# Optimization experiments

Hardware: AMD Instinct MI355X
Metric: run time of the kernel (lower is better)

Reference implementation:

```python
import jax, jax.numpy as jnp
import numpy as np

D_MODEL = 1024
NUM_HEADS = 16
NUM_KV_HEADS = 4
HEAD_DIM = D_MODEL // NUM_HEADS  # 64
THETA = 10000.0
MAX_SEQ_LEN = 4096


def _rope_tables(max_seq_len, d_k, theta):
    k_vec = jnp.arange(0, d_k, 2, dtype=jnp.float32) / d_k
    freq = 1.0 / (theta ** k_vec)                       # (d_k/2,)
    ang = jnp.arange(max_seq_len, dtype=jnp.float32)[:, None] * freq[None, :]
    return jnp.cos(ang), jnp.sin(ang)                   # each (max_seq_len, d_k/2)


def _apply_rope(x, pos, cos_table, sin_table):
    # x: (b, h, l, d), pos: (b, l)
    cos = cos_table[pos][:, None, :, :]                 # (b, 1, l, d/2)
    sin = sin_table[pos][:, None, :, :]
    even, odd = x[..., 0::2], x[..., 1::2]
    r1 = even * cos - odd * sin
    r2 = even * sin + odd * cos
    return jnp.stack([r1, r2], axis=-1).reshape(x.shape)  # interleave back


def setup_inputs() -> dict:
    key = jax.random.key(0)
    ks = jax.random.split(key, 6)
    B, L, D = 1, 4096, D_MODEL
    std = (2.0 / (D + D)) ** 0.5
    std_kv = (2.0 / (D + HEAD_DIM * NUM_KV_HEADS)) ** 0.5
    x = jax.random.normal(ks[0], (B, L, D), dtype=jnp.float32)
    Wq = jax.random.normal(ks[1], (D, D), dtype=jnp.float32) * std
    Wk = jax.random.normal(ks[2], (HEAD_DIM * NUM_KV_HEADS, D), dtype=jnp.float32) * std_kv
    Wv = jax.random.normal(ks[3], (HEAD_DIM * NUM_KV_HEADS, D), dtype=jnp.float32) * std_kv
    Wo = jax.random.normal(ks[4], (D, D), dtype=jnp.float32) * std
    token_positions = jnp.broadcast_to(jnp.arange(L, dtype=jnp.int32), (B, L))
    return {"x": x, "Wq": Wq, "Wk": Wk, "Wv": Wv, "Wo": Wo,
            "token_positions": token_positions}


def reference(x, Wq, Wk, Wv, Wo, token_positions):
    B, L, D = x.shape
    H, Hkv, Dh = NUM_HEADS, NUM_KV_HEADS, HEAD_DIM
    n_rep = H // Hkv
    cos_t, sin_t = _rope_tables(MAX_SEQ_LEN, Dh, THETA)

    q = (x @ Wq.T).reshape(B, L, H, Dh).transpose(0, 2, 1, 3)      # b h l d
    k = (x @ Wk.T).reshape(B, L, Hkv, Dh).transpose(0, 2, 1, 3)    # b g l d
    v = (x @ Wv.T).reshape(B, L, Hkv, Dh).transpose(0, 2, 1, 3)

    q = _apply_rope(q, token_positions, cos_t, sin_t)
    k = _apply_rope(k, token_positions, cos_t, sin_t)

    # GQA: group query heads by kv head
    qg = q.reshape(B, Hkv, n_rep, L, Dh)
    scores = jnp.einsum('bgrqd,bgkd->bgrqk', qg, k) / jnp.sqrt(jnp.float32(Dh))
    causal = jnp.tril(jnp.ones((L, L), dtype=bool))
    scores = jnp.where(causal, scores, -jnp.inf)
    weights = jax.nn.softmax(scores, axis=-1)
    out = jnp.einsum('bgrqk,bgkd->bgrqd', weights, v)              # b g r q d
    out = out.reshape(B, H, L, Dh).transpose(0, 2, 1, 3).reshape(B, L, D)
    return out @ Wo.T
```

## Files before the change

### kernel.cpp

```cpp
#include <hip/hip_runtime.h>
#include <hip/hip_bf16.h>
#include <math.h>

typedef __bf16 bf16;
typedef __bf16 v8bf __attribute__((ext_vector_type(8)));
typedef __bf16 v4bf __attribute__((ext_vector_type(4)));
typedef __bf16 v2bf __attribute__((ext_vector_type(2)));
typedef float f32x4 __attribute__((ext_vector_type(4)));
typedef float f32x16 __attribute__((ext_vector_type(16)));

#define L_SEQ 4096
#define DMODEL 1024
#define NHEADS 16
#define DH 64
#define NEG_BIG (-1e30f)
#define LN1E4_64 0.14391156f
#define SCL2 0.18033688f
#define DEFER_THR 8.0f

static __device__ __forceinline__ unsigned pkbf(float x, float y) {
    v2bf t; t[0] = (bf16)x; t[1] = (bf16)y;
    return __builtin_bit_cast(unsigned, t);
}

static __device__ __forceinline__ void gld16(const bf16* g, const bf16* l) {
    __builtin_amdgcn_global_load_lds((const __attribute__((address_space(1))) void*)g,
                                     (__attribute__((address_space(3))) void*)l, 16, 0, 0);
}

__global__ void convert_all(const float* __restrict__ x, const float* __restrict__ wq,
                            const float* __restrict__ wk, const float* __restrict__ wv,
                            const float* __restrict__ wo,
                            bf16* __restrict__ xb, bf16* __restrict__ wqkvb,
                            bf16* __restrict__ wob) {
    int i = (blockIdx.x * 256 + threadIdx.x) * 4;
    const float* src;
    bf16* dst;
    if (i < 4194304)      { src = x  + i;             dst = xb    + i; }
    else if (i < 5242880) { src = wq + (i - 4194304); dst = wqkvb + (i - 4194304); }
    else if (i < 5505024) { src = wk + (i - 5242880); dst = wqkvb + 1048576 + (i - 5242880); }
    else if (i < 5767168) { src = wv + (i - 5505024); dst = wqkvb + 1310720 + (i - 5505024); }
    else                  { src = wo + (i - 5767168); dst = wob   + (i - 5767168); }
    f32x4 v = *(const f32x4*)src;
    v4bf r;
#pragma unroll
    for (int j = 0; j < 4; j++) r[j] = (bf16)v[j];
    *(v4bf*)dst = r;
}

__global__ __launch_bounds__(512) void gemm_qkv(const bf16* __restrict__ A,
                                                const bf16* __restrict__ W,
                                                bf16* __restrict__ Qb,
                                                bf16* __restrict__ Kb,
                                                bf16* __restrict__ Vtg,
                                                const int* __restrict__ tp) {
    __shared__ bf16 As[2][128][64];
    __shared__ bf16 Bs[2][128][64];
    const int K = 1024;
    const int tid = threadIdx.x;
    const int w = tid >> 6, lane = tid & 63;
    const int quad = lane >> 4, l16 = lane & 15;
    const int wm = (w & 1) * 64, wn = (w >> 1) * 32;
    const int bm = blockIdx.x * 128, bn = blockIdx.y * 128;

    const int srow = lane >> 3;
    const int scol = ((lane & 7) ^ srow) << 3;

    f32x4 acc[4][2];
#pragma unroll
    for (int mf = 0; mf < 4; mf++)
#pragma unroll
        for (int nf = 0; nf < 2; nf++) acc[mf][nf] = (f32x4){0.f, 0.f, 0.f, 0.f};

#define QKV_STAGE(buf, ktt)                                                        \
    do {                                                                           \
        const bf16* ga = &A[(size_t)(bm + (w << 3) + srow) * 1024 + (ktt) + scol]; \
        const bf16* gb = &W[(size_t)(bn + (w << 3) + srow) * 1024 + (ktt) + scol]; \
        gld16(ga,             &As[buf][(w << 3)][0]);                              \
        gld16(ga + 64 * 1024, &As[buf][64 + (w << 3)][0]);                         \
        gld16(gb,             &Bs[buf][(w << 3)][0]);                              \
        gld16(gb + 64 * 1024, &Bs[buf][64 + (w << 3)][0]);                         \
    } while (0)

    QKV_STAGE(0, 0);
    __syncthreads();

    int cur = 0;
    for (int kt = 0; kt < K; kt += 64) {
        const bool more = (kt + 64) < K;
        if (more) QKV_STAGE(cur ^ 1, kt + 64);
#pragma unroll
        for (int kf = 0; kf < 2; kf++) {
            v8bf a[4], b[2];
#pragma unroll
            for (int mf = 0; mf < 4; mf++)
                a[mf] = *(v8bf*)&As[cur][wm + mf * 16 + l16][(((kf << 2) + quad) ^ (l16 & 7)) << 3];
#pragma unroll
            for (int nf = 0; nf < 2; nf++)
                b[nf] = *(v8bf*)&Bs[cur][wn + nf * 16 + l16][(((kf << 2) + quad) ^ (l16 & 7)) << 3];
#pragma unroll
            for (int mf = 0; mf < 4; mf++)
#pragma unroll
                for (int nf = 0; nf < 2; nf++)
                    acc[mf][nf] = __builtin_amdgcn_mfma_f32_16x16x32_bf16(a[mf], b[nf], acc[mf][nf], 0, 0, 0);
        }
        __syncthreads();
        cur ^= 1;
    }
#undef QKV_STAGE

    if (bn < 1024) {
#pragma unroll
        for (int mf = 0; mf < 4; mf++) {
            int pos_[4];
#pragma unroll
            for (int r = 0; r < 4; r++) pos_[r] = tp[bm + wm + mf * 16 + quad * 4 + r];
#pragma unroll
            for (int nf = 0; nf < 2; nf++) {
                const int col = bn + wn + nf * 16 + l16;
                float fr = __expf(-(float)((col & 63) & ~1) * LN1E4_64);
#pragma unroll
                for (int r = 0; r < 4; r++) {
                    float v = acc[mf][nf][r];
                    float sn, cs;
                    __sincosf((float)pos_[r] * fr, &sn, &cs);
                    float p = __shfl_xor(v, 1);
                    float res = (l16 & 1) ? (p * sn + v * cs) : (v * cs - p * sn);
                    int row = bm + wm + mf * 16 + quad * 4 + r;
                    Qb[(size_t)row * DMODEL + col] = (bf16)(res * SCL2);
                }
            }
        }
    } else if (bn < 1280) {
#pragma unroll
        for (int mf = 0; mf < 4; mf++) {
            int pos_[4];
#pragma unroll
            for (int r = 0; r < 4; r++) pos_[r] = tp[bm + wm + mf * 16 + quad * 4 + r];
#pragma unroll
            for (int nf = 0; nf < 2; nf++) {
                const int kcol = bn - 1024 + wn + nf * 16 + l16;
                float fr = __expf(-(float)((kcol & 63) & ~1) * LN1E4_64);
#pragma unroll
                for (int r = 0; r < 4; r++) {
                    float v = acc[mf][nf][r];
                    float sn, cs;
                    __sincosf((float)pos_[r] * fr, &sn, &cs);
                    float p = __shfl_xor(v, 1);
                    float res = (l16 & 1) ? (p * sn + v * cs) : (v * cs - p * sn);
                    int row = bm + wm + mf * 16 + quad * 4 + r;
                    Kb[(size_t)row * 256 + kcol] = (bf16)res;
                }
            }
        }
    } else {
#pragma unroll
        for (int mf = 0; mf < 4; mf++)
#pragma unroll
            for (int nf = 0; nf < 2; nf++) {
                v4bf pk;
#pragma unroll
                for (int r = 0; r < 4; r++) pk[r] = (bf16)acc[mf][nf][r];
                int vcol = bn - 1280 + wn + nf * 16 + l16;
                int row = bm + wm + mf * 16 + quad * 4;
                *(v4bf*)&Vtg[(size_t)vcol * L_SEQ + row] = pk;
            }
    }
}

__global__ __launch_bounds__(512) void gemm_out(const bf16* __restrict__ A,
                                                const bf16* __restrict__ W,
                                                float* __restrict__ C) {
    __shared__ bf16 As[2][128][64];
    __shared__ bf16 Bs[2][128][64];
    const int K = 1024, N = 1024;
    const int tid = threadIdx.x;
    const int w = tid >> 6, lane = tid & 63;
    const int quad = lane >> 4, l16 = lane & 15;
    const int wm = (w & 1) * 64, wn = (w >> 1) * 32;
    const int bm = blockIdx.x * 128, bn = blockIdx.y * 128;

    const int srow = lane >> 3;
    const int scol = ((lane & 7) ^ srow) << 3;

    f32x4 acc[4][2];
#pragma unroll
    for (int mf = 0; mf < 4; mf++)
#pragma unroll
        for (int nf = 0; nf < 2; nf++) acc[mf][nf] = (f32x4){0.f, 0.f, 0.f, 0.f};

#define OUT_STAGE(buf, ktt)                                                        \
    do {                                                                           \
        const bf16* ga = &A[(size_t)(bm + (w << 3) + srow) * 1024 + (ktt) + scol]; \
        const bf16* gb = &W[(size_t)(bn + (w << 3) + srow) * 1024 + (ktt) + scol]; \
        gld16(ga,             &As[buf][(w << 3)][0]);                              \
        gld16(ga + 64 * 1024, &As[buf][64 + (w << 3)][0]);                         \
        gld16(gb,             &Bs[buf][(w << 3)][0]);                              \
        gld16(gb + 64 * 1024, &Bs[buf][64 + (w << 3)][0]);                         \
    } while (0)

    OUT_STAGE(0, 0);
    __syncthreads();

    int cur = 0;
    for (int kt = 0; kt < K; kt += 64) {
        const bool more = (kt + 64) < K;
        if (more) OUT_STAGE(cur ^ 1, kt + 64);
#pragma unroll
        for (int kf = 0; kf < 2; kf++) {
            v8bf a[4], b[2];
#pragma unroll
            for (int mf = 0; mf < 4; mf++)
                a[mf] = *(v8bf*)&As[cur][wm + mf * 16 + l16][(((kf << 2) + quad) ^ (l16 & 7)) << 3];
#pragma unroll
            for (int nf = 0; nf < 2; nf++)
                b[nf] = *(v8bf*)&Bs[cur][wn + nf * 16 + l16][(((kf << 2) + quad) ^ (l16 & 7)) << 3];
#pragma unroll
            for (int mf = 0; mf < 4; mf++)
#pragma unroll
                for (int nf = 0; nf < 2; nf++)
                    acc[mf][nf] = __builtin_amdgcn_mfma_f32_16x16x32_bf16(a[mf], b[nf], acc[mf][nf], 0, 0, 0);
        }
        __syncthreads();
        cur ^= 1;
    }
#undef OUT_STAGE

#pragma unroll
    for (int mf = 0; mf < 4; mf++)
#pragma unroll
        for (int nf = 0; nf < 2; nf++)
#pragma unroll
            for (int r = 0; r < 4; r++) {
                int row = bm + wm + mf * 16 + quad * 4 + r;
                int col = bn + wn + nf * 16 + l16;
                C[(size_t)row * N + col] = acc[mf][nf][r];
            }
}

__global__ __launch_bounds__(256, 2) void flash11(const bf16* __restrict__ Q,
                                                  const bf16* __restrict__ Kb,
                                                  const bf16* __restrict__ Vtg,
                                                  bf16* __restrict__ O0,
                                                  bf16* __restrict__ O1,
                                                  float* __restrict__ ML) {
    __shared__ bf16 Ks[128][68];
    __shared__ bf16 Vt[64][132];
    const int h = blockIdx.x, kvh = h >> 2;
    const int bx = blockIdx.y;
    const int tid = threadIdx.x;
    const int w = tid >> 6, lane = tid & 63;
    const int l32 = lane & 31, hi = lane >> 5;
    const int krow = tid >> 1, kcb = (tid & 1) * 32;
    const int vr = tid >> 2, vcb = (tid & 3) * 32;

    v8bf ones;
#pragma unroll
    for (int j = 0; j < 8; j++) ones[j] = (bf16)1.0f;

    for (int p = 0; p < 2; p++) {
        const int qb = p ? (31 - bx) : bx;
        const int T = qb + 1;
        const int k0 = p ? ((T + 1) >> 1) : 0;
        const int k1 = p ? T : ((T + 1) >> 1);
        bf16* Op = p ? O1 : O0;
        float* mlp = ML + (size_t)(p * NHEADS + h) * L_SEQ * 2;

        if (k0 >= k1) {
            for (int i = tid; i < 128 * 64; i += 256) {
                int rr = i >> 6, cc = i & 63;
                Op[(size_t)(qb * 128 + rr) * DMODEL + h * DH + cc] = (bf16)0.f;
            }
            if (tid < 128) {
                mlp[(qb * 128 + tid) * 2 + 0] = NEG_BIG;
                mlp[(qb * 128 + tid) * 2 + 1] = 0.f;
            }
            continue;
        }

        const int qrow = qb * 128 + w * 32 + l32;
        v8bf qf[4];
#pragma unroll
        for (int d16 = 0; d16 < 4; d16++)
            qf[d16] = *(const v8bf*)&Q[(size_t)qrow * DMODEL + h * DH + d16 * 16 + hi * 8];

        f32x16 oaccT[2], lacc;
#pragma unroll
        for (int d = 0; d < 2; d++)
#pragma unroll
            for (int r = 0; r < 16; r++) oaccT[d][r] = 0.f;
#pragma unroll
        for (int r = 0; r < 16; r++) lacc[r] = 0.f;
        float m_i = NEG_BIG;

        v8bf kreg[4], vreg[4];
        {
            const bf16* ks = &Kb[(size_t)(k0 * 128 + krow) * 256 + kvh * DH + kcb];
            const bf16* vs = &Vtg[(size_t)(kvh * DH + vr) * L_SEQ + k0 * 128 + vcb];
#pragma unroll
            for (int u = 0; u < 4; u++) { kreg[u] = *(const v8bf*)&ks[8 * u]; vreg[u] = *(const v8bf*)&vs[8 * u]; }
            __syncthreads();
#pragma unroll
            for (int u = 0; u < 4; u++) { *(v8bf*)&Ks[krow][kcb + 8 * u] = kreg[u]; *(v8bf*)&Vt[vr][vcb + 8 * u] = vreg[u]; }
        }

        for (int kb = k0; kb < k1; kb++) {
            __syncthreads();
            if (kb + 1 < k1) {
                const bf16* ks = &Kb[(size_t)((kb + 1) * 128 + krow) * 256 + kvh * DH + kcb];
                const bf16* vs = &Vtg[(size_t)(kvh * DH + vr) * L_SEQ + (kb + 1) * 128 + vcb];
#pragma unroll
                for (int u = 0; u < 4; u++) { kreg[u] = *(const v8bf*)&ks[8 * u]; vreg[u] = *(const v8bf*)&vs[8 * u]; }
            }

            f32x16 s[4];
            __builtin_amdgcn_s_setprio(1);
#pragma unroll
            for (int n = 0; n < 4; n++) {
#pragma unroll
                for (int r = 0; r < 16; r++) s[n][r] = 0.f;
#pragma unroll
                for (int d16 = 0; d16 < 4; d16++) {
                    v8bf av = *(v8bf*)&Ks[n * 32 + l32][d16 * 16 + hi * 8];
                    s[n] = __builtin_amdgcn_mfma_f32_32x32x16_bf16(av, qf[d16], s[n], 0, 0, 0);
                }
            }
            __builtin_amdgcn_s_setprio(0);

            if (kb == qb) {
#pragma unroll
                for (int n = 0; n < 4; n++) {
                    int kbase = kb * 128 + n * 32 + 4 * hi;
#pragma unroll
                    for (int r = 0; r < 16; r++) {
                        int key = kbase + (r & 3) + 8 * (r >> 2);
                        if (key > qrow) s[n][r] = NEG_BIG;
                    }
                }
            }

            float mx = NEG_BIG;
#pragma unroll
            for (int n = 0; n < 4; n++)
#pragma unroll
                for (int r = 0; r < 16; r += 2)
                    mx = fmaxf(fmaxf(mx, s[n][r]), s[n][r + 1]);
            mx = fmaxf(mx, __shfl_xor(mx, 32));

            if (!__all(mx <= m_i + DEFER_THR)) {
                float mnew = fmaxf(m_i, mx);
                float alpha = exp2f(m_i - mnew);
#pragma unroll
                for (int r = 0; r < 16; r++) lacc[r] *= alpha;
#pragma unroll
                for (int d = 0; d < 2; d++)
#pragma unroll
                    for (int r = 0; r < 16; r++) oaccT[d][r] *= alpha;
                m_i = mnew;
            }

#pragma unroll
            for (int n = 0; n < 4; n++)
#pragma unroll
                for (int r = 0; r < 16; r++)
                    s[n][r] = exp2f(s[n][r] - m_i);

            __builtin_amdgcn_s_setprio(1);
#pragma unroll
            for (int n = 0; n < 4; n++) {
#pragma unroll
                for (int u = 0; u < 2; u++) {
                    const int ro = u * 8;
                    unsigned a0 = pkbf(s[n][ro + 0], s[n][ro + 1]);
                    unsigned a1 = pkbf(s[n][ro + 2], s[n][ro + 3]);
                    unsigned b0 = pkbf(s[n][ro + 4], s[n][ro + 5]);
                    unsigned b1 = pkbf(s[n][ro + 6], s[n][ro + 7]);
#if __has_builtin(__builtin_amdgcn_permlane32_swap)
                    auto s0 = __builtin_amdgcn_permlane32_swap(a0, b0, false, false);
                    auto s1 = __builtin_amdgcn_permlane32_swap(a1, b1, false, false);
                    unsigned w0 = s0[0], w2 = s0[1], w1 = s1[0], w3 = s1[1];
#else
                    unsigned t0 = hi ? a0 : b0;
                    unsigned r0 = __shfl_xor(t0, 32);
                    unsigned w0 = hi ? r0 : a0, w2 = hi ? b0 : r0;
                    unsigned t1 = hi ? a1 : b1;
                    unsigned r1 = __shfl_xor(t1, 32);
                    unsigned w1 = hi ? r1 : a1, w3 = hi ? b1 : r1;
#endif
                    union { unsigned uu[4]; v8bf v; } pf;
                    pf.uu[0] = w0; pf.uu[1] = w1; pf.uu[2] = w2; pf.uu[3] = w3;
                    const int t = n * 2 + u;
#pragma unroll
                    for (int dblk = 0; dblk < 2; dblk++) {
                        v8bf av = *(v8bf*)&Vt[dblk * 32 + l32][t * 16 + hi * 8];
                        oaccT[dblk] = __builtin_amdgcn_mfma_f32_32x32x16_bf16(av, pf.v, oaccT[dblk], 0, 0, 0);
                    }
                    lacc = __builtin_amdgcn_mfma_f32_32x32x16_bf16(ones, pf.v, lacc, 0, 0, 0);
                }
            }
            __builtin_amdgcn_s_setprio(0);

            __syncthreads();
            if (kb + 1 < k1) {
#pragma unroll
                for (int u = 0; u < 4; u++) { *(v8bf*)&Ks[krow][kcb + 8 * u] = kreg[u]; *(v8bf*)&Vt[vr][vcb + 8 * u] = vreg[u]; }
            }
        }

#pragma unroll
        for (int dblk = 0; dblk < 2; dblk++)
#pragma unroll
            for (int r = 0; r < 16; r++) {
                int d = dblk * 32 + (r & 3) + 8 * (r >> 2) + 4 * hi;
                Ks[w * 32 + l32][d] = (bf16)oaccT[dblk][r];
            }
        asm volatile("s_waitcnt lgkmcnt(0)" ::: "memory");
        __builtin_amdgcn_sched_barrier(0);
#pragma unroll
        for (int i = 0; i < 4; i++) {
            int cc = (lane & 1) * 32 + i * 8;
            int rr = w * 32 + (lane >> 1);
            v8bf ov = *(v8bf*)&Ks[rr][cc];
            *(v8bf*)&Op[(size_t)(qb * 128 + rr) * DMODEL + h * DH + cc] = ov;
        }
        if (hi == 0) {
            mlp[qrow * 2 + 0] = m_i;
            mlp[qrow * 2 + 1] = lacc[0];
        }
    }
}

__global__ void combine(const bf16* __restrict__ O0, const bf16* __restrict__ O1,
                        const float* __restrict__ ML, bf16* __restrict__ Attn) {
    int gid = blockIdx.x * 256 + threadIdx.x;
    int row = gid >> 8;
    int cg = (gid & 255) * 4;
    int h = cg >> 6;
    const float* ml0 = ML + ((size_t)h * L_SEQ + row) * 2;
    const float* ml1 = ML + ((size_t)(NHEADS + h) * L_SEQ + row) * 2;
    float m0 = ml0[0], l0 = ml0[1], m1 = ml1[0], l1 = ml1[1];
    float m = fmaxf(m0, m1);
    float a0 = exp2f(m0 - m), a1 = exp2f(m1 - m);
    float inv = 1.f / (a0 * l0 + a1 * l1);
    v4bf o0 = *(const v4bf*)&O0[(size_t)row * DMODEL + cg];
    v4bf o1 = *(const v4bf*)&O1[(size_t)row * DMODEL + cg];
    v4bf res;
#pragma unroll
    for (int j = 0; j < 4; j++)
        res[j] = (bf16)((a0 * (float)o0[j] + a1 * (float)o1[j]) * inv);
    *(v4bf*)&Attn[(size_t)row * DMODEL + cg] = res;
}

extern "C" void kernel_launch(void* const* d_in, const int* in_sizes, int n_in,
                              void* d_out, int out_size, void* d_ws, size_t ws_size,
                              hipStream_t stream) {
    const float* x  = (const float*)d_in[0];
    const float* Wq = (const float*)d_in[1];
    const float* Wk = (const float*)d_in[2];
    const float* Wv = (const float*)d_in[3];
    const float* Wo = (const float*)d_in[4];
    const int*   tp = (const int*)d_in[5];
    float* out = (float*)d_out;

    bf16*  xb    = (bf16*)d_ws;
    bf16*  wqkvb = xb    + 4194304;
    bf16*  wob   = wqkvb + 1572864;
    bf16*  Qb    = wob   + 1048576;
    bf16*  Kb    = Qb    + 4194304;
    bf16*  Vtg   = Kb    + 1048576;
    float* MLf   = (float*)(Vtg + 1048576);
    bf16*  Attn  = xb;
    bf16*  O0    = (bf16*)d_out;
    bf16*  O1    = O0 + 4194304;

    convert_all<<<6656, 256, 0, stream>>>(x, Wq, Wk, Wv, Wo, xb, wqkvb, wob);
    gemm_qkv<<<dim3(32, 12), 512, 0, stream>>>(xb, wqkvb, Qb, Kb, Vtg, tp);
    flash11<<<dim3(NHEADS, 32), 256, 0, stream>>>(Qb, Kb, Vtg, O0, O1, MLf);
    combine<<<4096, 256, 0, stream>>>(O0, O1, MLf, Attn);
    gemm_out<<<dim3(32, 8), 512, 0, stream>>>(Attn, wob, out);
}
```

Before: 194.7 us.

## Drop split-KV partials and combine kernel, normalize attention output in flash

The attention kernel no longer splits each query block's key range into two halves that are merged later. Each pass now walks keys from zero up to the causal limit, divides by the row sum in registers, and writes normalized bf16 output straight into the Attn buffer. This removes the combine launch and the traffic for the partial outputs and max/sum values. However, the grid still pairs bx with 31-bx, so every query block is now computed by two different blocks. That roughly doubles the attention math and K/V traffic per block.

```diff
diff --git a/kernel.cpp b/kernel.cpp
--- a/kernel.cpp
+++ b/kernel.cpp
@@ -238,12 +238,10 @@
             }
 }
 
-__global__ __launch_bounds__(256, 2) void flash11(const bf16* __restrict__ Q,
+__global__ __launch_bounds__(256, 2) void flash14(const bf16* __restrict__ Q,
                                                   const bf16* __restrict__ Kb,
                                                   const bf16* __restrict__ Vtg,
-                                                  bf16* __restrict__ O0,
-                                                  bf16* __restrict__ O1,
-                                                  float* __restrict__ ML) {
+                                                  bf16* __restrict__ Attn) {
     __shared__ bf16 Ks[128][68];
     __shared__ bf16 Vt[64][132];
     const int h = blockIdx.x, kvh = h >> 2;
@@ -260,23 +258,7 @@
 
     for (int p = 0; p < 2; p++) {
         const int qb = p ? (31 - bx) : bx;
-        const int T = qb + 1;
-        const int k0 = p ? ((T + 1) >> 1) : 0;
-        const int k1 = p ? T : ((T + 1) >> 1);
-        bf16* Op = p ? O1 : O0;
-        float* mlp = ML + (size_t)(p * NHEADS + h) * L_SEQ * 2;
-
-        if (k0 >= k1) {
-            for (int i = tid; i < 128 * 64; i += 256) {
-                int rr = i >> 6, cc = i & 63;
-                Op[(size_t)(qb * 128 + rr) * DMODEL + h * DH + cc] = (bf16)0.f;
-            }
-            if (tid < 128) {
-                mlp[(qb * 128 + tid) * 2 + 0] = NEG_BIG;
-                mlp[(qb * 128 + tid) * 2 + 1] = 0.f;
-            }
-            continue;
-        }
+        const int k1 = qb + 1;
 
         const int qrow = qb * 128 + w * 32 + l32;
         v8bf qf[4];
@@ -295,8 +277,8 @@
 
         v8bf kreg[4], vreg[4];
         {
-            const bf16* ks = &Kb[(size_t)(k0 * 128 + krow) * 256 + kvh * DH + kcb];
-            const bf16* vs = &Vtg[(size_t)(kvh * DH + vr) * L_SEQ + k0 * 128 + vcb];
+            const bf16* ks = &Kb[(size_t)krow * 256 + kvh * DH + kcb];
+            const bf16* vs = &Vtg[(size_t)(kvh * DH + vr) * L_SEQ + vcb];
 #pragma unroll
             for (int u = 0; u < 4; u++) { kreg[u] = *(const v8bf*)&ks[8 * u]; vreg[u] = *(const v8bf*)&vs[8 * u]; }
             __syncthreads();
@@ -304,7 +286,7 @@
             for (int u = 0; u < 4; u++) { *(v8bf*)&Ks[krow][kcb + 8 * u] = kreg[u]; *(v8bf*)&Vt[vr][vcb + 8 * u] = vreg[u]; }
         }
 
-        for (int kb = k0; kb < k1; kb++) {
+        for (int kb = 0; kb < k1; kb++) {
             __syncthreads();
             if (kb + 1 < k1) {
                 const bf16* ks = &Kb[(size_t)((kb + 1) * 128 + krow) * 256 + kvh * DH + kcb];
@@ -407,48 +389,24 @@
             }
         }
 
+        const float linv = 1.f / lacc[0];
 #pragma unroll
         for (int dblk = 0; dblk < 2; dblk++)
 #pragma unroll
             for (int r = 0; r < 16; r++) {
                 int d = dblk * 32 + (r & 3) + 8 * (r >> 2) + 4 * hi;
-                Ks[w * 32 + l32][d] = (bf16)oaccT[dblk][r];
+                Ks[w * 32 + l32][d] = (bf16)(oaccT[dblk][r] * linv);
             }
         asm volatile("s_waitcnt lgkmcnt(0)" ::: "memory");
         __builtin_amdgcn_sched_barrier(0);
 #pragma unroll
-        for (int i = 0; i < 4; i++) {
-            int cc = (lane & 1) * 32 + i * 8;
+        for (int ii = 0; ii < 4; ii++) {
+            int cc = (lane & 1) * 32 + ii * 8;
             int rr = w * 32 + (lane >> 1);
             v8bf ov = *(v8bf*)&Ks[rr][cc];
-            *(v8bf*)&Op[(size_t)(qb * 128 + rr) * DMODEL + h * DH + cc] = ov;
-        }
-        if (hi == 0) {
-            mlp[qrow * 2 + 0] = m_i;
-            mlp[qrow * 2 + 1] = lacc[0];
+            *(v8bf*)&Attn[(size_t)(qb * 128 + rr) * DMODEL + h * DH + cc] = ov;
         }
     }
-}
-
-__global__ void combine(const bf16* __restrict__ O0, const bf16* __restrict__ O1,
-                        const float* __restrict__ ML, bf16* __restrict__ Attn) {
-    int gid = blockIdx.x * 256 + threadIdx.x;
-    int row = gid >> 8;
-    int cg = (gid & 255) * 4;
-    int h = cg >> 6;
-    const float* ml0 = ML + ((size_t)h * L_SEQ + row) * 2;
-    const float* ml1 = ML + ((size_t)(NHEADS + h) * L_SEQ + row) * 2;
-    float m0 = ml0[0], l0 = ml0[1], m1 = ml1[0], l1 = ml1[1];
-    float m = fmaxf(m0, m1);
-    float a0 = exp2f(m0 - m), a1 = exp2f(m1 - m);
-    float inv = 1.f / (a0 * l0 + a1 * l1);
-    v4bf o0 = *(const v4bf*)&O0[(size_t)row * DMODEL + cg];
-    v4bf o1 = *(const v4bf*)&O1[(size_t)row * DMODEL + cg];
-    v4bf res;
-#pragma unroll
-    for (int j = 0; j < 4; j++)
-        res[j] = (bf16)((a0 * (float)o0[j] + a1 * (float)o1[j]) * inv);
-    *(v4bf*)&Attn[(size_t)row * DMODEL + cg] = res;
 }
 
 extern "C" void kernel_launch(void* const* d_in, const int* in_sizes, int n_in,
@@ -468,14 +426,10 @@
     bf16*  Qb    = wob   + 1048576;
     bf16*  Kb    = Qb    + 4194304;
     bf16*  Vtg   = Kb    + 1048576;
-    float* MLf   = (float*)(Vtg + 1048576);
-    bf16*  Attn  = xb;
-    bf16*  O0    = (bf16*)d_out;
-    bf16*  O1    = O0 + 4194304;
+    bf16*  Attn  = Vtg   + 1048576;
 
     convert_all<<<6656, 256, 0, stream>>>(x, Wq, Wk, Wv, Wo, xb, wqkvb, wob);
     gemm_qkv<<<dim3(32, 12), 512, 0, stream>>>(xb, wqkvb, Qb, Kb, Vtg, tp);
-    flash11<<<dim3(NHEADS, 32), 256, 0, stream>>>(Qb, Kb, Vtg, O0, O1, MLf);
-    combine<<<4096, 256, 0, stream>>>(O0, O1, MLf, Attn);
+    flash14<<<dim3(NHEADS, 32), 256, 0, stream>>>(Qb, Kb, Vtg, Attn);
     gemm_out<<<dim3(32, 8), 512, 0, stream>>>(Attn, wob, out);
 }
```

Result: slower. 239.5 us (+23.0%).
